# Kernel tuning notes

Measured on AMD Instinct MI355X. Metric: run time of the kernel, lower is better.

Reference implementation:

```python
import jax, jax.numpy as jnp
import numpy as np

N_NODES = 50000
N_EDGES = 800000
D = 128          # d_model
N_LAYER = 4
N_GRAPHS = 128
N_IDS = 256      # nn.Embedding(256, d_model)


def setup_inputs() -> dict:
    key = jax.random.key(0)
    ks = jax.random.split(key, 10)
    s = 0.02
    return {
        "position_feature": jax.random.normal(ks[0], (N_NODES, 3), dtype=jnp.float32),
        "id_feature": jax.random.randint(ks[1], (N_NODES,), 0, N_IDS),
        "edge_index": jax.random.randint(ks[2], (2, N_EDGES), 0, N_NODES),
        "batch": jnp.sort(jax.random.randint(ks[3], (N_NODES,), 0, N_GRAPHS)),
        "num_graphs": N_GRAPHS,
        "Wp": jax.random.normal(ks[4], (3, D), dtype=jnp.float32) * s,
        "bp": jnp.zeros((D,), jnp.float32),
        "id_emb": jax.random.normal(ks[5], (N_IDS, D), dtype=jnp.float32) * s,
        "Wn": jax.random.normal(ks[6], (2 * D, D), dtype=jnp.float32) * s,
        "bn": jnp.zeros((D,), jnp.float32),
        "conv_W": jax.random.normal(ks[7], (N_LAYER, D, D), dtype=jnp.float32) * s,
        "conv_b": jnp.zeros((N_LAYER, D), jnp.float32),
        "Wa": jax.random.normal(ks[8], ((1 + N_LAYER) * D, D), dtype=jnp.float32) * s,
        "ba": jnp.zeros((D,), jnp.float32),
    }


def _gcn(x, W, b, src, dst, norm, n):
    # PyG GCNConv: h = x @ W; out[dst] += norm(e) * h[src]; out += bias
    h = x @ W
    msg = h[src] * norm[:, None]
    return jax.ops.segment_sum(msg, dst, num_segments=n) + b


def reference(position_feature, id_feature, edge_index, batch, num_graphs,
              Wp, bp, id_emb, Wn, bn, conv_W, conv_b, Wa, ba):
    n = position_feature.shape[0]
    # GCN normalization with self-loops (shared across all layers)
    loops = jnp.arange(n)
    src = jnp.concatenate([edge_index[0], loops])
    dst = jnp.concatenate([edge_index[1], loops])
    deg = jax.ops.segment_sum(jnp.ones_like(src, dtype=position_feature.dtype), dst, num_segments=n)
    dinv = jnp.where(deg > 0, jax.lax.rsqrt(deg), 0.0)
    norm = dinv[src] * dinv[dst]  # [E + N]

    pos = jax.nn.relu(position_feature @ Wp + bp)       # [N, D]
    idf = jax.nn.relu(id_emb[id_feature])               # [N, D]
    x = jax.nn.relu(jnp.concatenate([pos, idf], axis=1) @ Wn + bn)  # [N, D]

    gs = [jax.ops.segment_max(x, batch, num_segments=num_graphs)]   # g_embed_0
    h = x
    for l in range(conv_W.shape[0]):
        h = jax.nn.relu(_gcn(h, conv_W[l], conv_b[l], src, dst, norm, n))
        gs.append(jax.ops.segment_max(h, batch, num_segments=num_graphs))

    g_embed = jnp.concatenate(gs, axis=1)  # [G, (1+n_layer)*D]
    return g_embed @ Wa + ba               # [G, D]
```

## Files before the change

kernel.cpp:

```cpp
#include <hip/hip_runtime.h>

#define N_NODES 50000
#define N_EDGES 800000
#define D 128
#define NLAYER 4
#define NGRAPH 128
#define GDIM (5 * D)
#define NBUCK 196
#define BCAP 4608

typedef __attribute__((ext_vector_type(8))) short bf16x8;
typedef __attribute__((ext_vector_type(4))) float f32x4;

__device__ __forceinline__ float b2f(unsigned short u) {
    return __uint_as_float(((unsigned)u) << 16);
}
__device__ __forceinline__ unsigned short f2b(float f) {
    unsigned u = __float_as_uint(f);
    unsigned r = (u + 0x7fffu + ((u >> 16) & 1u)) >> 16;
    return (unsigned short)r;
}


__global__ __launch_bounds__(256) void k_bucket(
    const int* __restrict__ esrc, const int* __restrict__ edst,
    int* __restrict__ cnt, int* __restrict__ bcnt_rel, int* __restrict__ ebuf) {
    __shared__ int hcnt[NBUCK];
    __shared__ int hbase[NBUCK];
    int t = threadIdx.x;
    for (int i = t; i < NBUCK; i += 256) hcnt[i] = 0;
    __syncthreads();
    int e0 = blockIdx.x * 2048 + t;
    int d[8], s[8];
#pragma unroll
    for (int i = 0; i < 8; ++i) {
        int e = e0 + i * 256;
        if (e < N_EDGES) {
            d[i] = edst[e];
            s[i] = esrc[e];
            atomicAdd(&cnt[d[i]], 1);
            atomicAdd(&hcnt[d[i] >> 8], 1);
        } else {
            d[i] = -1;
        }
    }
    __syncthreads();
    for (int i = t; i < NBUCK; i += 256) {
        int c = hcnt[i];
        hbase[i] = (c > 0) ? (i * BCAP + atomicAdd(&bcnt_rel[i], c)) : 0;
        hcnt[i] = 0;
    }
    __syncthreads();
#pragma unroll
    for (int i = 0; i < 8; ++i) {
        if (d[i] >= 0) {
            int b = d[i] >> 8;
            int p = atomicAdd(&hcnt[b], 1);
            int pos = hbase[b] + p;
            if (pos < (b + 1) * BCAP)
                ebuf[pos] = (s[i] & 0xffff) | ((d[i] & 255) << 16);
        }
    }
}


__global__ void k_scanA(const int* __restrict__ cnt, int* __restrict__ offs,
                        int* __restrict__ chunkSum) {
    __shared__ int lds[256];
    int tid = threadIdx.x;
    int base = blockIdx.x * 1024 + tid * 4;
    int v[4];
    int s = 0;
#pragma unroll
    for (int j = 0; j < 4; ++j) {
        int idx = base + j;
        v[j] = (idx < N_NODES) ? cnt[idx] : 0;
        s += v[j];
    }
    lds[tid] = s;
    __syncthreads();
    int t = s;
    for (int off = 1; off < 256; off <<= 1) {
        int add = (tid >= off) ? lds[tid - off] : 0;
        __syncthreads();
        t += add;
        lds[tid] = t;
        __syncthreads();
    }
    int run = t - s;
#pragma unroll
    for (int j = 0; j < 4; ++j) {
        int idx = base + j;
        if (idx < N_NODES) offs[idx] = run;
        run += v[j];
    }
    if (tid == 255) chunkSum[blockIdx.x] = t;
}

__global__ void k_scanB(const int* __restrict__ chunkSum, int* __restrict__ chunkOff,
                        int nc) {
    __shared__ int lds[64];
    int tid = threadIdx.x;
    int v = (tid < nc) ? chunkSum[tid] : 0;
    lds[tid] = v;
    __syncthreads();
    int t = v;
    for (int off = 1; off < 64; off <<= 1) {
        int add = (tid >= off) ? lds[tid - off] : 0;
        __syncthreads();
        t += add;
        lds[tid] = t;
        __syncthreads();
    }
    if (tid < nc) chunkOff[tid] = t - v;
}

__global__ void k_scanC(int* __restrict__ offs, const int* __restrict__ chunkOff,
                        const int* __restrict__ cnt, float* __restrict__ dinv,
                        const int* __restrict__ batch, int* __restrict__ hist2) {
    int i = blockIdx.x * 256 + threadIdx.x;
    if (i < N_NODES) {
        offs[i] += chunkOff[i >> 10];
        int c = cnt[i];
        dinv[i] = 1.f / sqrtf((float)(c + 1));
        atomicAdd(&hist2[batch[i] * 128 + min(c, 127)], 1);
    }
}

__global__ __launch_bounds__(1024) void k_scan16k(int* __restrict__ hist2) {
    __shared__ int lds[1024];
    int t = threadIdx.x;
    int v[16];
    int s = 0;
#pragma unroll
    for (int j = 0; j < 16; ++j) { v[j] = hist2[t * 16 + j]; s += v[j]; }
    lds[t] = s;
    __syncthreads();
    int tot = s;
    for (int off = 1; off < 1024; off <<= 1) {
        int add = (t >= off) ? lds[t - off] : 0;
        __syncthreads();
        tot += add;
        lds[t] = tot;
        __syncthreads();
    }
    int run = tot - s;
#pragma unroll
    for (int j = 0; j < 16; ++j) { hist2[t * 16 + j] = run; run += v[j]; }
}

__global__ void k_scatter(const int* __restrict__ cnt, const int* __restrict__ batch,
                          int* __restrict__ hist2, int* __restrict__ perm) {
    int i = blockIdx.x * 256 + threadIdx.x;
    if (i < N_NODES) {
        int key = batch[i] * 128 + min(cnt[i], 127);
        int p = atomicAdd(&hist2[key], 1);
        perm[p] = i;
    }
}

__global__ __launch_bounds__(256) void k_fillB(
    const int* __restrict__ ebuf, const int* __restrict__ bcnt_rel,
    const int* __restrict__ offs, const float* __restrict__ dinv,
    unsigned int* __restrict__ csrs) {
    __shared__ int loffs[256];
    __shared__ int lcnt[256];
    __shared__ float ldinv[256];
    int b = blockIdx.x, t = threadIdx.x;
    int nbase = b << 8;
    if (nbase + t < N_NODES) {
        loffs[t] = offs[nbase + t];
        ldinv[t] = dinv[nbase + t];
    }
    lcnt[t] = 0;
    __syncthreads();
    int s0 = b * BCAP, s1 = b * BCAP + bcnt_rel[b];
    for (int i = s0 + t; i < s1; i += 256) {
        int pk = ebuf[i];
        int ld = (pk >> 16) & 255;
        int src = pk & 0xffff;
        float w = dinv[src] * ldinv[ld];
        int p = atomicAdd(&lcnt[ld], 1);
        csrs[loffs[ld] + p] = (unsigned)src | ((unsigned)f2b(w) << 16);
    }
}


__global__ __launch_bounds__(256) void k_prep(
    const float* __restrict__ Wn, const float* __restrict__ convW,
    unsigned short* __restrict__ Wpack,
    const float* __restrict__ id_emb, float* __restrict__ T) {
    int blk = blockIdx.x;
    if (blk < 320) {
        int tid = blk * 256 + threadIdx.x;
        int m = tid >> 14;
        int rem = tid & 16383;
        int ct = rem >> 11, kc = (rem >> 9) & 3, l = (rem >> 3) & 63, j = rem & 7;
        int k = kc * 32 + ((l >> 4) * 8) + j;
        int n = ct * 16 + (l & 15);
        const float* src = (m == 0) ? Wn : (convW + (size_t)(m - 1) * 16384);
        Wpack[tid] = f2b(src[k * 128 + n]);
    } else {
        int t = threadIdx.x;
        int d = t & 127;
        int r = (blk - 320) * 2 + (t >> 7);
        float acc = 0.f;
        for (int k = 0; k < 128; ++k)
            acc = fmaf(fmaxf(id_emb[r * 128 + k], 0.f), Wn[(128 + k) * 128 + d], acc);
        T[r * 128 + d] = acc;
    }
}


__global__ __launch_bounds__(256) void k_encoder(
    const float* __restrict__ pos, const int* __restrict__ idfeat,
    const float* __restrict__ Wp, const float* __restrict__ bp,
    const unsigned short* __restrict__ WpackE, const float* __restrict__ bn,
    const float* __restrict__ T, unsigned short* __restrict__ A16,
    const int* __restrict__ batch, float* __restrict__ gbuf) {
    __shared__ unsigned short feat[64 * 128];
    __shared__ float posl[192];
    __shared__ int bbat[64];
    int t = threadIdx.x;
    int base = blockIdx.x * 64;
    int avail = N_NODES - base;
    if (t < 192) {
        int idx = base * 3 + t;
        posl[t] = (idx < N_NODES * 3) ? pos[idx] : 0.f;
    }
    if (t < 64) bbat[t] = (base + t < N_NODES) ? batch[base + t] : -1;
    __syncthreads();
#pragma unroll
    for (int i = 0; i < 4; ++i) {
        int gid = t + i * 256;
        int row = gid >> 4, kg = gid & 15;
        unsigned short u[8];
        if (row < avail) {
            float p0 = posl[row * 3], p1 = posl[row * 3 + 1], p2 = posl[row * 3 + 2];
#pragma unroll
            for (int j = 0; j < 8; ++j) {
                int d = kg * 8 + j;
                float v = fmaf(p0, Wp[d], fmaf(p1, Wp[128 + d], fmaf(p2, Wp[256 + d], bp[d])));
                u[j] = f2b(fmaxf(v, 0.f));
            }
        } else {
#pragma unroll
            for (int j = 0; j < 8; ++j) u[j] = 0;
        }
        char* dst = (char*)feat + row * 256 + ((kg * 16) ^ ((row & 7) << 4));
        *(uint4*)dst = *(uint4*)u;
    }
    __syncthreads();
    int wid = t >> 6, l = t & 63;
    int r0 = wid * 16;
    f32x4 acc[8];
#pragma unroll
    for (int ct = 0; ct < 8; ++ct) acc[ct] = (f32x4){0.f, 0.f, 0.f, 0.f};
    const bf16x8* wp = (const bf16x8*)WpackE;
#pragma unroll
    for (int kc = 0; kc < 4; ++kc) {
        int row = r0 + (l & 15);
        const char* ap = (const char*)feat + row * 256 +
                         ((kc * 64 + ((l >> 4) * 16)) ^ ((row & 7) << 4));
        bf16x8 afrag = *(const bf16x8*)ap;
#pragma unroll
        for (int ct = 0; ct < 8; ++ct) {
            bf16x8 bfrag = wp[(ct * 4 + kc) * 64 + l];
            acc[ct] = __builtin_amdgcn_mfma_f32_16x16x32_bf16(afrag, bfrag, acc[ct], 0, 0, 0);
        }
    }
    int subrow = (l >> 4) * 4, col0 = l & 15;
    int ids[4];
#pragma unroll
    for (int i = 0; i < 4; ++i) {
        int node = base + r0 + subrow + i;
        ids[i] = (node < N_NODES) ? idfeat[node] : 0;
    }
    __syncthreads();
#pragma unroll
    for (int ct = 0; ct < 8; ++ct) {
        int col = ct * 16 + col0;
        float bcol = bn[col];
#pragma unroll
        for (int i = 0; i < 4; ++i) {
            int node = base + r0 + subrow + i;
            unsigned short ob = 0;
            if (node < N_NODES) {
                float v = acc[ct][i] + bcol + T[ids[i] * 128 + col];
                ob = f2b(fmaxf(v, 0.f));
                A16[(size_t)node * 128 + col] = ob;
            }
            feat[(r0 + subrow + i) * 128 + col] = ob;
        }
    }
    __syncthreads();
    if (t < 128) {
        int j = 0;
        while (j < 64) {
            int g = bbat[j];
            float m = b2f(feat[j * 128 + t]);
            int k = j + 1;
            while (k < 64 && bbat[k] == g) { m = fmaxf(m, b2f(feat[k * 128 + t])); ++k; }
            if (g >= 0) atomicMax((int*)&gbuf[g * GDIM + t], __float_as_int(m));
            j = k;
        }
    }
}


__global__ __launch_bounds__(512) void k_layer(
    const unsigned short* __restrict__ Hin, unsigned short* __restrict__ Hout,
    const unsigned short* __restrict__ WpackL,
    const int* __restrict__ offs, const int* __restrict__ cnt,
    const unsigned int* __restrict__ csrs, const float* __restrict__ dinv,
    const float* __restrict__ bias, const int* __restrict__ batch,
    const int* __restrict__ perm, float* __restrict__ gbuf, int goff) {
    __shared__ unsigned short hagg[16 * 128];
    __shared__ float smx[16][132];
    __shared__ int bb[16];
    __shared__ int snode[16];
    int tid = threadIdx.x;
    int wave = tid >> 6, lane = tid & 63;
    int sub = lane >> 5, l = lane & 31;
    int row = wave * 2 + sub;
    int nbase = blockIdx.x * 16;
    if (tid < 16) {
        int n = perm[nbase + tid];
        snode[tid] = n;
        bb[tid] = batch[n];
    }
    int node = perm[nbase + row];

    int start = offs[node];
    int c = cnt[node];
    float di = dinv[node];
    float sw = di * di;
    const ushort4* B4 = (const ushort4*)Hin;
    ushort4 sv = B4[(size_t)node * 32 + l];
    float4 acc;
    acc.x = sw * b2f(sv.x);
    acc.y = sw * b2f(sv.y);
    acc.z = sw * b2f(sv.z);
    acc.w = sw * b2f(sv.w);
    int j = 0;
    for (; j + 8 <= c; j += 8) {
        unsigned pk[8];
        ushort4 v[8];
#pragma unroll
        for (int i = 0; i < 8; ++i) pk[i] = csrs[start + j + i];
#pragma unroll
        for (int i = 0; i < 8; ++i) v[i] = B4[(size_t)(pk[i] & 0xffffu) * 32 + l];
#pragma unroll
        for (int i = 0; i < 8; ++i) {
            float w = __uint_as_float(pk[i] & 0xffff0000u);
            acc.x = fmaf(w, b2f(v[i].x), acc.x);
            acc.y = fmaf(w, b2f(v[i].y), acc.y);
            acc.z = fmaf(w, b2f(v[i].z), acc.z);
            acc.w = fmaf(w, b2f(v[i].w), acc.w);
        }
    }
    for (; j < c; ++j) {
        unsigned pk = csrs[start + j];
        float w = __uint_as_float(pk & 0xffff0000u);
        ushort4 v = B4[(size_t)(pk & 0xffffu) * 32 + l];
        acc.x = fmaf(w, b2f(v.x), acc.x);
        acc.y = fmaf(w, b2f(v.y), acc.y);
        acc.z = fmaf(w, b2f(v.z), acc.z);
        acc.w = fmaf(w, b2f(v.w), acc.w);
    }
    {
        unsigned short u[4] = {f2b(acc.x), f2b(acc.y), f2b(acc.z), f2b(acc.w)};
        char* dst = (char*)hagg + row * 256 + ((((l >> 1) * 16) ^ ((row & 7) << 4)) + (l & 1) * 8);
        *(uint2*)dst = *(uint2*)u;
    }
    __syncthreads();

    f32x4 oacc = (f32x4){0.f, 0.f, 0.f, 0.f};
    const bf16x8* wp = (const bf16x8*)WpackL;
#pragma unroll
    for (int kc = 0; kc < 4; ++kc) {
        int arow = lane & 15;
        const char* ap = (const char*)hagg + arow * 256 +
                         ((kc * 64 + ((lane >> 4) * 16)) ^ ((arow & 7) << 4));
        bf16x8 afrag = *(const bf16x8*)ap;
        bf16x8 bfrag = wp[(wave * 4 + kc) * 64 + lane];
        oacc = __builtin_amdgcn_mfma_f32_16x16x32_bf16(afrag, bfrag, oacc, 0, 0, 0);
    }

    int col = wave * 16 + (lane & 15);
    int subrow = (lane >> 4) * 4;
    float bcol = bias[col];
#pragma unroll
    for (int i = 0; i < 4; ++i) {
        int r = subrow + i;
        float v = fmaxf(oacc[i] + bcol, 0.f);
        smx[r][col] = v;
        Hout[(size_t)snode[r] * 128 + col] = f2b(v);
    }
    __syncthreads();
    if (tid < 128) {
        int jj = 0;
        while (jj < 16) {
            int g = bb[jj];
            float m = smx[jj][tid];
            int k = jj + 1;
            while (k < 16 && bb[k] == g) { m = fmaxf(m, smx[k][tid]); ++k; }
            atomicMax((int*)&gbuf[g * GDIM + goff + tid], __float_as_int(m));
            jj = k;
        }
    }
}


__global__ __launch_bounds__(128) void k_final(const float* __restrict__ gbuf,
                                               const float* __restrict__ Wa,
                                               const float* __restrict__ ba,
                                               float* __restrict__ out) {
    __shared__ float gr[GDIM];
    int g = blockIdx.x, t = threadIdx.x;
    for (int i = t; i < GDIM; i += 128) gr[i] = gbuf[g * GDIM + i];
    __syncthreads();
    float acc = ba[t];
    for (int k = 0; k < GDIM; ++k) acc = fmaf(gr[k], Wa[k * 128 + t], acc);
    out[g * 128 + t] = acc;
}


extern "C" void kernel_launch(void* const* d_in, const int* in_sizes, int n_in,
                              void* d_out, int out_size, void* d_ws, size_t ws_size,
                              hipStream_t stream) {
    const float* pos    = (const float*)d_in[0];
    const int*   idfeat = (const int*)d_in[1];
    const int*   eidx   = (const int*)d_in[2];
    const int*   batch  = (const int*)d_in[3];
    const float* Wp     = (const float*)d_in[5];
    const float* bp     = (const float*)d_in[6];
    const float* id_emb = (const float*)d_in[7];
    const float* Wn     = (const float*)d_in[8];
    const float* bn     = (const float*)d_in[9];
    const float* convW  = (const float*)d_in[10];
    const float* convb  = (const float*)d_in[11];
    const float* Wa     = (const float*)d_in[12];
    const float* ba     = (const float*)d_in[13];
    float* out = (float*)d_out;

    const int* esrc = eidx;
    const int* edst = eidx + N_EDGES;

    char* w = (char*)d_ws;
    auto alloc = [&](size_t bytes) -> char* {
        char* p = w;
        w += (bytes + 255) & ~(size_t)255;
        return p;
    };
    char* zstart = w;
    int*   cnt      = (int*)alloc((size_t)N_NODES * 4);
    float* gbuf     = (float*)alloc((size_t)NGRAPH * GDIM * 4);
    int*   hist2    = (int*)alloc((size_t)16384 * 4);
    int*   bcnt_rel = (int*)alloc((size_t)NBUCK * 4);
    size_t zbytes = (size_t)(w - zstart);

    unsigned short* A16a = (unsigned short*)alloc((size_t)N_NODES * D * 2);
    unsigned short* A16b = (unsigned short*)alloc((size_t)N_NODES * D * 2);
    float* dinv = (float*)alloc((size_t)N_NODES * 4);
    int*   offs = (int*)alloc((size_t)(N_NODES + 1) * 4);
    int*   csum = (int*)alloc(64 * 4);
    int*   coff = (int*)alloc(64 * 4);
    unsigned int* csrs = (unsigned int*)alloc((size_t)N_EDGES * 4);
    int*   ebuf = (int*)alloc((size_t)NBUCK * BCAP * 4);
    int*   perm = (int*)alloc((size_t)N_NODES * 4);
    float* T    = (float*)alloc((size_t)256 * D * 4);
    unsigned short* Wpack = (unsigned short*)alloc((size_t)5 * 16384 * 2);

    hipMemsetAsync(zstart, 0, zbytes, stream);

    k_bucket<<<(N_EDGES + 2047) / 2048, 256, 0, stream>>>(esrc, edst, cnt, bcnt_rel, ebuf);

    int nchunk = (N_NODES + 1023) / 1024;
    k_scanA<<<nchunk, 256, 0, stream>>>(cnt, offs, csum);
    k_scanB<<<1, 64, 0, stream>>>(csum, coff, nchunk);
    k_scanC<<<(N_NODES + 255) / 256, 256, 0, stream>>>(offs, coff, cnt, dinv, batch, hist2);
    k_scan16k<<<1, 1024, 0, stream>>>(hist2);
    k_scatter<<<(N_NODES + 255) / 256, 256, 0, stream>>>(cnt, batch, hist2, perm);

    k_fillB<<<NBUCK, 256, 0, stream>>>(ebuf, bcnt_rel, offs, dinv, csrs);

    k_prep<<<448, 256, 0, stream>>>(Wn, convW, Wpack, id_emb, T);
    k_encoder<<<(N_NODES + 63) / 64, 256, 0, stream>>>(pos, idfeat, Wp, bp, Wpack, bn, T,
                                                       A16a, batch, gbuf);

    unsigned short* Hin = A16a;
    unsigned short* Hout = A16b;
    for (int l = 0; l < NLAYER; ++l) {
        k_layer<<<N_NODES / 16, 512, 0, stream>>>(Hin, Hout, Wpack + (size_t)(l + 1) * 16384,
                                                  offs, cnt, csrs, dinv,
                                                  convb + (size_t)l * D, batch, perm, gbuf,
                                                  (l + 1) * D);
        unsigned short* tmp = Hin; Hin = Hout; Hout = tmp;
    }

    k_final<<<NGRAPH, 128, 0, stream>>>(gbuf, Wa, ba, out);
}
```

Baseline: 288.7 us.

## Halve layer block size: 16 lanes per node row with 16-byte gathers

The GCN layer kernel now runs 256 threads per block instead of 512. Each node row is handled by 16 lanes that each gather 8 bf16 values with one 16-byte load, rather than 32 lanes doing 8-byte loads. Each wave then computes two 16-column MFMA output tiles instead of one. This cuts thread count and instruction overhead per gathered edge and widens memory transactions, at the cost of more registers per thread and fewer lanes in flight to hide gather latency.

New measurement: 281.1 us. 1.03x faster.

```diff
diff --git a/kernel.cpp b/kernel.cpp
--- a/kernel.cpp
+++ b/kernel.cpp
@@ -308,7 +308,7 @@
 }
 
 
-__global__ __launch_bounds__(512) void k_layer(
+__global__ __launch_bounds__(256) void k_layer(
     const unsigned short* __restrict__ Hin, unsigned short* __restrict__ Hout,
     const unsigned short* __restrict__ WpackL,
     const int* __restrict__ offs, const int* __restrict__ cnt,
@@ -321,8 +321,8 @@
     __shared__ int snode[16];
     int tid = threadIdx.x;
     int wave = tid >> 6, lane = tid & 63;
-    int sub = lane >> 5, l = lane & 31;
-    int row = wave * 2 + sub;
+    int q = lane >> 4, l16 = lane & 15;
+    int row = wave * 4 + q;
     int nbase = blockIdx.x * 16;
     if (tid < 16) {
         int n = perm[nbase + tid];
@@ -335,47 +335,64 @@
     int c = cnt[node];
     float di = dinv[node];
     float sw = di * di;
-    const ushort4* B4 = (const ushort4*)Hin;
-    ushort4 sv = B4[(size_t)node * 32 + l];
-    float4 acc;
-    acc.x = sw * b2f(sv.x);
-    acc.y = sw * b2f(sv.y);
-    acc.z = sw * b2f(sv.z);
-    acc.w = sw * b2f(sv.w);
+    const uint4* B4 = (const uint4*)Hin;
+    float a[8];
+    {
+        uint4 sv = B4[(size_t)node * 16 + l16];
+        a[0] = sw * __uint_as_float(sv.x << 16);
+        a[1] = sw * __uint_as_float(sv.x & 0xffff0000u);
+        a[2] = sw * __uint_as_float(sv.y << 16);
+        a[3] = sw * __uint_as_float(sv.y & 0xffff0000u);
+        a[4] = sw * __uint_as_float(sv.z << 16);
+        a[5] = sw * __uint_as_float(sv.z & 0xffff0000u);
+        a[6] = sw * __uint_as_float(sv.w << 16);
+        a[7] = sw * __uint_as_float(sv.w & 0xffff0000u);
+    }
     int j = 0;
     for (; j + 8 <= c; j += 8) {
         unsigned pk[8];
-        ushort4 v[8];
+        uint4 v[8];
 #pragma unroll
         for (int i = 0; i < 8; ++i) pk[i] = csrs[start + j + i];
 #pragma unroll
-        for (int i = 0; i < 8; ++i) v[i] = B4[(size_t)(pk[i] & 0xffffu) * 32 + l];
+        for (int i = 0; i < 8; ++i) v[i] = B4[(size_t)(pk[i] & 0xffffu) * 16 + l16];
 #pragma unroll
         for (int i = 0; i < 8; ++i) {
             float w = __uint_as_float(pk[i] & 0xffff0000u);
-            acc.x = fmaf(w, b2f(v[i].x), acc.x);
-            acc.y = fmaf(w, b2f(v[i].y), acc.y);
-            acc.z = fmaf(w, b2f(v[i].z), acc.z);
-            acc.w = fmaf(w, b2f(v[i].w), acc.w);
+            a[0] = fmaf(w, __uint_as_float(v[i].x << 16), a[0]);
+            a[1] = fmaf(w, __uint_as_float(v[i].x & 0xffff0000u), a[1]);
+            a[2] = fmaf(w, __uint_as_float(v[i].y << 16), a[2]);
+            a[3] = fmaf(w, __uint_as_float(v[i].y & 0xffff0000u), a[3]);
+            a[4] = fmaf(w, __uint_as_float(v[i].z << 16), a[4]);
+            a[5] = fmaf(w, __uint_as_float(v[i].z & 0xffff0000u), a[5]);
+            a[6] = fmaf(w, __uint_as_float(v[i].w << 16), a[6]);
+            a[7] = fmaf(w, __uint_as_float(v[i].w & 0xffff0000u), a[7]);
         }
     }
     for (; j < c; ++j) {
         unsigned pk = csrs[start + j];
         float w = __uint_as_float(pk & 0xffff0000u);
-        ushort4 v = B4[(size_t)(pk & 0xffffu) * 32 + l];
-        acc.x = fmaf(w, b2f(v.x), acc.x);
-        acc.y = fmaf(w, b2f(v.y), acc.y);
-        acc.z = fmaf(w, b2f(v.z), acc.z);
-        acc.w = fmaf(w, b2f(v.w), acc.w);
+        uint4 v = B4[(size_t)(pk & 0xffffu) * 16 + l16];
+        a[0] = fmaf(w, __uint_as_float(v.x << 16), a[0]);
+        a[1] = fmaf(w, __uint_as_float(v.x & 0xffff0000u), a[1]);
+        a[2] = fmaf(w, __uint_as_float(v.y << 16), a[2]);
+        a[3] = fmaf(w, __uint_as_float(v.y & 0xffff0000u), a[3]);
+        a[4] = fmaf(w, __uint_as_float(v.z << 16), a[4]);
+        a[5] = fmaf(w, __uint_as_float(v.z & 0xffff0000u), a[5]);
+        a[6] = fmaf(w, __uint_as_float(v.w << 16), a[6]);
+        a[7] = fmaf(w, __uint_as_float(v.w & 0xffff0000u), a[7]);
     }
     {
-        unsigned short u[4] = {f2b(acc.x), f2b(acc.y), f2b(acc.z), f2b(acc.w)};
-        char* dst = (char*)hagg + row * 256 + ((((l >> 1) * 16) ^ ((row & 7) << 4)) + (l & 1) * 8);
-        *(uint2*)dst = *(uint2*)u;
-    }
-    __syncthreads();
-
-    f32x4 oacc = (f32x4){0.f, 0.f, 0.f, 0.f};
+        unsigned u[4];
+#pragma unroll
+        for (int k = 0; k < 4; ++k)
+            u[k] = (unsigned)f2b(a[2 * k]) | ((unsigned)f2b(a[2 * k + 1]) << 16);
+        char* dst = (char*)hagg + row * 256 + ((l16 * 16) ^ ((row & 7) << 4));
+        *(uint4*)dst = *(uint4*)u;
+    }
+    __syncthreads();
+
+    f32x4 oacc[2] = {(f32x4){0.f, 0.f, 0.f, 0.f}, (f32x4){0.f, 0.f, 0.f, 0.f}};
     const bf16x8* wp = (const bf16x8*)WpackL;
 #pragma unroll
     for (int kc = 0; kc < 4; ++kc) {
@@ -383,19 +400,26 @@
         const char* ap = (const char*)hagg + arow * 256 +
                          ((kc * 64 + ((lane >> 4) * 16)) ^ ((arow & 7) << 4));
         bf16x8 afrag = *(const bf16x8*)ap;
-        bf16x8 bfrag = wp[(wave * 4 + kc) * 64 + lane];
-        oacc = __builtin_amdgcn_mfma_f32_16x16x32_bf16(afrag, bfrag, oacc, 0, 0, 0);
-    }
-
-    int col = wave * 16 + (lane & 15);
+#pragma unroll
+        for (int ci = 0; ci < 2; ++ci) {
+            int ct = wave * 2 + ci;
+            bf16x8 bfrag = wp[(ct * 4 + kc) * 64 + lane];
+            oacc[ci] = __builtin_amdgcn_mfma_f32_16x16x32_bf16(afrag, bfrag, oacc[ci], 0, 0, 0);
+        }
+    }
+
     int subrow = (lane >> 4) * 4;
-    float bcol = bias[col];
-#pragma unroll
-    for (int i = 0; i < 4; ++i) {
-        int r = subrow + i;
-        float v = fmaxf(oacc[i] + bcol, 0.f);
-        smx[r][col] = v;
-        Hout[(size_t)snode[r] * 128 + col] = f2b(v);
+#pragma unroll
+    for (int ci = 0; ci < 2; ++ci) {
+        int col = (wave * 2 + ci) * 16 + (lane & 15);
+        float bcol = bias[col];
+#pragma unroll
+        for (int i = 0; i < 4; ++i) {
+            int r = subrow + i;
+            float v = fmaxf(oacc[ci][i] + bcol, 0.f);
+            smx[r][col] = v;
+            Hout[(size_t)snode[r] * 128 + col] = f2b(v);
+        }
     }
     __syncthreads();
     if (tid < 128) {
@@ -492,7 +516,7 @@
     unsigned short* Hin = A16a;
     unsigned short* Hout = A16b;
     for (int l = 0; l < NLAYER; ++l) {
-        k_layer<<<N_NODES / 16, 512, 0, stream>>>(Hin, Hout, Wpack + (size_t)(l + 1) * 16384,
+        k_layer<<<N_NODES / 16, 256, 0, stream>>>(Hin, Hout, Wpack + (size_t)(l + 1) * 16384,
                                                   offs, cnt, csrs, dinv,
                                                   convb + (size_t)l * D, batch, perm, gbuf,
                                                   (l + 1) * D);
```
